# Optimization experiments

Measured on AMD Instinct MI355X. Metric: run time of the kernel, lower is better.

Reference implementation:

```python
import jax, jax.numpy as jnp
import numpy as np

WEIGHT = 0.1
EPS = 1e-8


def setup_inputs() -> dict:
    key = jax.random.key(0)
    # [B, 3, D, H, W] deformation field
    deformation_field = jax.random.normal(key, (2, 3, 192, 192, 192), dtype=jnp.float32)
    return {"deformation_field": deformation_field}


def reference(deformation_field):
    f = deformation_field
    # jnp.gradient matches torch.gradient defaults: 2nd-order central interior,
    # 1st-order one-sided differences at the edges, unit spacing.
    grad_x = jnp.gradient(f, axis=2)
    grad_y = jnp.gradient(f, axis=3)
    grad_z = jnp.gradient(f, axis=4)

    divergence = grad_x[:, 0:1] + grad_y[:, 1:2] + grad_z[:, 2:3]
    divergence_loss = jnp.mean(divergence ** 2)

    curl_x = grad_z[:, 1:2] - grad_y[:, 2:3]
    curl_y = grad_x[:, 2:3] - grad_z[:, 0:1]
    curl_z = grad_y[:, 0:1] - grad_x[:, 1:2]
    curl_magnitude = jnp.sqrt(curl_x ** 2 + curl_y ** 2 + curl_z ** 2 + EPS)
    curl_loss = jnp.mean(curl_magnitude)

    return WEIGHT * (divergence_loss + curl_loss)
```

## Files before the change

### kernel.cpp

```cpp
#include <hip/hip_runtime.h>


#define DEP 192
#define HGT 192
#define WID 192
#define NB  2

constexpr int SD = HGT * WID;
constexpr int SC = DEP * SD;
constexpr int SB = 3 * SC;
constexpr int DSEG = 12;
constexpr int NSEG = DEP / DSEG;
constexpr int RPB  = 4;
constexpr int NRPG = (HGT / 2) / RPB;
constexpr int NBLK = NB * NSEG * NRPG;
constexpr float SCALE = (float)(0.1 / (double)((long long)NB * DEP * HGT * WID));
constexpr float EPS_C = 1e-8f;

struct V3 { float x, y, z; };
__device__ __forceinline__ V3 ld3(const float* p) {
    const float3 t = *(const float3*)p;
    V3 r; r.x = t.x; r.y = t.y; r.z = t.z; return r;
}

__global__ __launch_bounds__(256, 3) void gcl_kernel(const float* __restrict__ f,
                                                     float* __restrict__ ws) {
    const int tid  = threadIdx.x;
    const int lane = tid & 63;
    const int wv   = tid >> 6;

    int bid = blockIdx.x;
    const int rpg = bid % NRPG; bid /= NRPG;
    const int dsg = bid % NSEG;
    const int b   = bid / NSEG;

    const int h0 = (rpg * RPB + wv) * 2;
    const int h1 = h0 + 1;
    const int w  = lane * 3;
    const int d0 = dsg * DSEG;

    const int hmrow = (h0 > 0) ? h0 - 1 : 0;
    const int hprow = (h1 < HGT - 1) ? h1 + 1 : HGT - 1;
    const float sy0 = (h0 == 0) ? 1.f : 0.5f;
    const float sy1 = (h1 == HGT - 1) ? 1.f : 0.5f;
    const float s0w = (lane == 0) ? 1.f : 0.5f;
    const float s2w = (lane == 63) ? 1.f : 0.5f;

    const float* base = f + b * SB + w;
    const int r0 = h0 * WID, r1 = h1 * WID, rm = hmrow * WID, rp = hprow * WID;

    V3 prev[3][2], cur[3][2], nxt[3][2], hm[3], hp[3];
    const int pm = (d0 > 0) ? d0 - 1 : 0;
#pragma unroll
    for (int c = 0; c < 3; ++c) {
        const float* pc = base + c * SC;
        prev[c][0] = ld3(pc + pm * SD + r0);
        prev[c][1] = ld3(pc + pm * SD + r1);
        cur[c][0]  = ld3(pc + d0 * SD + r0);
        cur[c][1]  = ld3(pc + d0 * SD + r1);
        nxt[c][0]  = ld3(pc + (d0 + 1) * SD + r0);
        nxt[c][1]  = ld3(pc + (d0 + 1) * SD + r1);
        hm[c]      = ld3(pc + d0 * SD + rm);
        hp[c]      = ld3(pc + d0 * SD + rp);
    }

    float local = 0.f;

#pragma unroll
    for (int s = 0; s < DSEG; ++s) {
        const int d = d0 + s;

        V3 nn[3][2], nhm[3], nhp[3];
        if (s < DSEG - 1) {
            const int dn = d + 1;
            const int d2 = (d + 2 < DEP) ? d + 2 : DEP - 1;
#pragma unroll
            for (int c = 0; c < 3; ++c) {
                const float* pc = base + c * SC;
                nn[c][0] = ld3(pc + d2 * SD + r0);
                nn[c][1] = ld3(pc + d2 * SD + r1);
                nhm[c]   = ld3(pc + dn * SD + rm);
                nhp[c]   = ld3(pc + dn * SD + rp);
            }
        }

        const float sx = (d == 0 || d == DEP - 1) ? 1.f : 0.5f;

#pragma unroll
        for (int r = 0; r < 2; ++r) {
            const float syr = r ? sy1 : sy0;
            float gx[3][3], gy[3][3], gz[3][3];
#pragma unroll
            for (int c = 0; c < 3; ++c) {
                gx[c][0] = sx * (nxt[c][r].x - prev[c][r].x);
                gx[c][1] = sx * (nxt[c][r].y - prev[c][r].y);
                gx[c][2] = sx * (nxt[c][r].z - prev[c][r].z);
                const V3 lo = r ? cur[c][0] : hm[c];
                const V3 hi = r ? hp[c]     : cur[c][1];
                gy[c][0] = syr * (hi.x - lo.x);
                gy[c][1] = syr * (hi.y - lo.y);
                gy[c][2] = syr * (hi.z - lo.z);
                float lv = __shfl_up(cur[c][r].z, 1, 64);
                float rv = __shfl_down(cur[c][r].x, 1, 64);
                if (lane == 0)  lv = cur[c][r].x;
                if (lane == 63) rv = cur[c][r].z;
                gz[c][0] = s0w * (cur[c][r].y - lv);
                gz[c][1] = 0.5f * (cur[c][r].z - cur[c][r].x);
                gz[c][2] = s2w * (rv - cur[c][r].y);
            }
#pragma unroll
            for (int j = 0; j < 3; ++j) {
                const float dv = gx[0][j] + gy[1][j] + gz[2][j];
                const float cx = gz[1][j] - gy[2][j];
                const float cy = gx[2][j] - gz[0][j];
                const float cz = gy[0][j] - gx[1][j];
                local += dv * dv +
                         __builtin_amdgcn_sqrtf(cx * cx + cy * cy + cz * cz + EPS_C);
            }
        }

        if (s < DSEG - 1) {
#pragma unroll
            for (int c = 0; c < 3; ++c) {
                prev[c][0] = cur[c][0]; prev[c][1] = cur[c][1];
                cur[c][0]  = nxt[c][0]; cur[c][1]  = nxt[c][1];
                nxt[c][0]  = nn[c][0];  nxt[c][1]  = nn[c][1];
                hm[c] = nhm[c]; hp[c] = nhp[c];
            }
        }
    }

#pragma unroll
    for (int off = 32; off > 0; off >>= 1)
        local += __shfl_down(local, off, 64);

    __shared__ float wsum[4];
    if (lane == 0) wsum[wv] = local;
    __syncthreads();
    if (tid == 0)
        ws[blockIdx.x] = wsum[0] + wsum[1] + wsum[2] + wsum[3];
}

__global__ __launch_bounds__(256) void gcl_reduce(const float* __restrict__ ws,
                                                  float* __restrict__ out) {
    float s = 0.f;
    for (int i = threadIdx.x; i < NBLK; i += 256) s += ws[i];
#pragma unroll
    for (int off = 32; off > 0; off >>= 1)
        s += __shfl_down(s, off, 64);
    __shared__ float wsum[4];
    const int lane = threadIdx.x & 63;
    const int wv   = threadIdx.x >> 6;
    if (lane == 0) wsum[wv] = s;
    __syncthreads();
    if (threadIdx.x == 0)
        out[0] = (wsum[0] + wsum[1] + wsum[2] + wsum[3]) * SCALE;
}

extern "C" void kernel_launch(void* const* d_in, const int* in_sizes, int n_in,
                              void* d_out, int out_size, void* d_ws, size_t ws_size,
                              hipStream_t stream) {
    const float* f = (const float*)d_in[0];
    float* out = (float*)d_out;
    float* ws  = (float*)d_ws;
    gcl_kernel<<<dim3(NBLK), dim3(256), 0, stream>>>(f, ws);
    gcl_reduce<<<dim3(1), dim3(256), 0, stream>>>(ws, out);
}
```

Baseline: 234.1 us.

## Share neighbor H-rows via LDS instead of reloading halo rows per wave

Each wave writes its two current rows into a double-buffered shared-memory tile every depth step, and neighboring waves read their H-direction neighbors from it. Only the edge waves still load halo rows from global memory. This is meant to cut the redundant global traffic from every wave loading two extra rows per step. In exchange it adds a block-wide barrier per depth step, extra LDS stores and loads, and more divergent code paths.

```diff
diff --git a/kernel.cpp b/kernel.cpp
--- a/kernel.cpp
+++ b/kernel.cpp
@@ -23,6 +23,20 @@
     V3 r; r.x = t.x; r.y = t.y; r.z = t.z; return r;
 }
 
+__device__ __forceinline__ void pack9(float* q, const V3 a0, const V3 a1, const V3 a2) {
+    ((float4*)q)[0] = make_float4(a0.x, a0.y, a0.z, a1.x);
+    ((float4*)q)[1] = make_float4(a1.y, a1.z, a2.x, a2.y);
+    q[8] = a2.z;
+}
+__device__ __forceinline__ void unpack9(const float* q, V3 v[3]) {
+    const float4 a = ((const float4*)q)[0];
+    const float4 b = ((const float4*)q)[1];
+    const float  c = q[8];
+    v[0] = {a.x, a.y, a.z};
+    v[1] = {a.w, b.x, b.y};
+    v[2] = {b.z, b.w, c};
+}
+
 __global__ __launch_bounds__(256, 3) void gcl_kernel(const float* __restrict__ f,
                                                      float* __restrict__ ws) {
     const int tid  = threadIdx.x;
@@ -49,7 +63,10 @@
     const float* base = f + b * SB + w;
     const int r0 = h0 * WID, r1 = h1 * WID, rm = hmrow * WID, rp = hprow * WID;
 
-    V3 prev[3][2], cur[3][2], nxt[3][2], hm[3], hp[3];
+    __shared__ float sh[2][2 * RPB][64][12];
+
+    V3 prev[3][2], cur[3][2], nxt[3][2];
+    V3 hm[3] = {}, hp[3] = {};
     const int pm = (d0 > 0) ? d0 - 1 : 0;
 #pragma unroll
     for (int c = 0; c < 3; ++c) {
@@ -60,8 +77,14 @@
         cur[c][1]  = ld3(pc + d0 * SD + r1);
         nxt[c][0]  = ld3(pc + (d0 + 1) * SD + r0);
         nxt[c][1]  = ld3(pc + (d0 + 1) * SD + r1);
-        hm[c]      = ld3(pc + d0 * SD + rm);
-        hp[c]      = ld3(pc + d0 * SD + rp);
+    }
+    if (wv == 0) {
+#pragma unroll
+        for (int c = 0; c < 3; ++c) hm[c] = ld3(base + c * SC + d0 * SD + rm);
+    }
+    if (wv == RPB - 1) {
+#pragma unroll
+        for (int c = 0; c < 3; ++c) hp[c] = ld3(base + c * SC + d0 * SD + rp);
     }
 
     float local = 0.f;
@@ -69,6 +92,10 @@
 #pragma unroll
     for (int s = 0; s < DSEG; ++s) {
         const int d = d0 + s;
+        const int p = s & 1;
+
+        pack9(&sh[p][2 * wv + 0][lane][0], cur[0][0], cur[1][0], cur[2][0]);
+        pack9(&sh[p][2 * wv + 1][lane][0], cur[0][1], cur[1][1], cur[2][1]);
 
         V3 nn[3][2], nhm[3], nhp[3];
         if (s < DSEG - 1) {
@@ -79,27 +106,44 @@
                 const float* pc = base + c * SC;
                 nn[c][0] = ld3(pc + d2 * SD + r0);
                 nn[c][1] = ld3(pc + d2 * SD + r1);
-                nhm[c]   = ld3(pc + dn * SD + rm);
-                nhp[c]   = ld3(pc + dn * SD + rp);
+            }
+            if (wv == 0) {
+#pragma unroll
+                for (int c = 0; c < 3; ++c) nhm[c] = ld3(base + c * SC + dn * SD + rm);
+            }
+            if (wv == RPB - 1) {
+#pragma unroll
+                for (int c = 0; c < 3; ++c) nhp[c] = ld3(base + c * SC + dn * SD + rp);
             }
         }
+
+        __syncthreads();
 
         const float sx = (d == 0 || d == DEP - 1) ? 1.f : 0.5f;
 
 #pragma unroll
         for (int r = 0; r < 2; ++r) {
             const float syr = r ? sy1 : sy0;
+            V3 lo3[3], hi3[3];
+            if (r == 0) {
+                if (wv == 0) { lo3[0] = hm[0]; lo3[1] = hm[1]; lo3[2] = hm[2]; }
+                else         unpack9(&sh[p][2 * wv - 1][lane][0], lo3);
+                hi3[0] = cur[0][1]; hi3[1] = cur[1][1]; hi3[2] = cur[2][1];
+            } else {
+                lo3[0] = cur[0][0]; lo3[1] = cur[1][0]; lo3[2] = cur[2][0];
+                if (wv == RPB - 1) { hi3[0] = hp[0]; hi3[1] = hp[1]; hi3[2] = hp[2]; }
+                else               unpack9(&sh[p][2 * wv + 2][lane][0], hi3);
+            }
+
             float gx[3][3], gy[3][3], gz[3][3];
 #pragma unroll
             for (int c = 0; c < 3; ++c) {
                 gx[c][0] = sx * (nxt[c][r].x - prev[c][r].x);
                 gx[c][1] = sx * (nxt[c][r].y - prev[c][r].y);
                 gx[c][2] = sx * (nxt[c][r].z - prev[c][r].z);
-                const V3 lo = r ? cur[c][0] : hm[c];
-                const V3 hi = r ? hp[c]     : cur[c][1];
-                gy[c][0] = syr * (hi.x - lo.x);
-                gy[c][1] = syr * (hi.y - lo.y);
-                gy[c][2] = syr * (hi.z - lo.z);
+                gy[c][0] = syr * (hi3[c].x - lo3[c].x);
+                gy[c][1] = syr * (hi3[c].y - lo3[c].y);
+                gy[c][2] = syr * (hi3[c].z - lo3[c].z);
                 float lv = __shfl_up(cur[c][r].z, 1, 64);
                 float rv = __shfl_down(cur[c][r].x, 1, 64);
                 if (lane == 0)  lv = cur[c][r].x;
@@ -125,7 +169,14 @@
                 prev[c][0] = cur[c][0]; prev[c][1] = cur[c][1];
                 cur[c][0]  = nxt[c][0]; cur[c][1]  = nxt[c][1];
                 nxt[c][0]  = nn[c][0];  nxt[c][1]  = nn[c][1];
-                hm[c] = nhm[c]; hp[c] = nhp[c];
+            }
+            if (wv == 0) {
+#pragma unroll
+                for (int c = 0; c < 3; ++c) hm[c] = nhm[c];
+            }
+            if (wv == RPB - 1) {
+#pragma unroll
+                for (int c = 0; c < 3; ++c) hp[c] = nhp[c];
             }
         }
     }
```

Measured after the change: 702.9 us. 3x slower.
